# Kernel tuning notes

Hardware: AMD Instinct MI355X
Metric: run time of the kernel (lower is better)

Reference implementation:

```python
import jax, jax.numpy as jnp
import numpy as np

B, T, D, UNITS = 64, 2048, 512, 512


def setup_inputs() -> dict:
    key = jax.random.key(0)
    ks = jax.random.split(key, 6)
    scale = 1.0 / np.sqrt(D)
    return {
        "features": jax.random.normal(ks[0], (B, T, D), dtype=jnp.float32),
        "hidden": jax.random.normal(ks[1], (B, D), dtype=jnp.float32),
        "W1_w": jax.random.normal(ks[2], (D, UNITS), dtype=jnp.float32) * scale,
        "W1_b": jnp.zeros((UNITS,), dtype=jnp.float32),
        "W2_w": jax.random.normal(ks[3], (D, UNITS), dtype=jnp.float32) * scale,
        "W2_b": jnp.zeros((UNITS,), dtype=jnp.float32),
        "V_w": jax.random.normal(ks[4], (UNITS, 1), dtype=jnp.float32) * (1.0 / np.sqrt(UNITS)),
        "V_b": jnp.zeros((1,), dtype=jnp.float32),
    }


def reference(features, hidden, W1_w, W1_b, W2_w, W2_b, V_w, V_b):
    # features: [B, T, D], hidden: [B, D]
    f_proj = jnp.einsum("btd,du->btu", features, W1_w) + W1_b      # [B, T, U]
    h_proj = (hidden @ W2_w + W2_b)[:, None, :]                     # [B, 1, U]
    score = jnp.tanh(f_proj + h_proj) @ V_w + V_b                   # [B, T, 1]
    attn = jax.nn.softmax(score, axis=1)                            # softmax over time
    context = jnp.sum(attn * features, axis=1)                      # [B, D]
    return context
```

## Files before the change

kernel.cpp:

```cpp
#include <hip/hip_runtime.h>
#include <hip/hip_bf16.h>

#define B_DIM 64
#define T_DIM 2048
#define D_DIM 512
#define U_DIM 512

typedef __bf16 bf16x8 __attribute__((ext_vector_type(8)));
typedef float  f32x4  __attribute__((ext_vector_type(4)));
typedef unsigned int u32;

__device__ __forceinline__ void gl_lds16(const __bf16* g, __bf16* l) {
    __builtin_amdgcn_global_load_lds(
        (const __attribute__((address_space(1))) u32*)g,
        (__attribute__((address_space(3))) u32*)l,
        16, 0, 0);
}

__global__ void w1s_kernel(const float* __restrict__ W1w, __bf16* __restrict__ w1s) {
    __shared__ float tile[64][33];
    const int tid = threadIdx.x;
    const int kb2 = blockIdx.x;
    const int ub  = blockIdx.y;
    #pragma unroll
    for (int i = 0; i < 8; ++i) {
        int k = i * 4 + (tid >> 6);
        int u = tid & 63;
        tile[u][k] = W1w[(kb2 * 32 + k) * U_DIM + ub * 64 + u];
    }
    __syncthreads();
    int u_l = tid >> 2;
    int kp  = (tid & 3) * 8;
    bf16x8 w;
    #pragma unroll
    for (int j = 0; j < 8; ++j) w[j] = (__bf16)tile[u_l][kp + j];
    *reinterpret_cast<bf16x8*>(&w1s[kb2 * 16384 + (ub * 64 + u_l) * 32 + kp]) = w;
}

__global__ void hproj_kernel(const float* __restrict__ hidden,
                             const float* __restrict__ W2w,
                             const float* __restrict__ W2b,
                             const float* __restrict__ W1b,
                             float* __restrict__ hp) {
    int b = blockIdx.x;
    int u = blockIdx.y * 256 + threadIdx.x;
    float acc = W2b[u] + W1b[u];
    const float* hrow = hidden + b * D_DIM;
    #pragma unroll 8
    for (int d = 0; d < D_DIM; ++d)
        acc = fmaf(hrow[d], W2w[d * U_DIM + u], acc);
    hp[b * U_DIM + u] = acc;
}

__global__ __launch_bounds__(256, 2) void score_ctx_kernel(
        const float*  __restrict__ features,
        const __bf16* __restrict__ w1s,
        const float*  __restrict__ hp,
        const float*  __restrict__ Vw,
        float*        __restrict__ ctx,
        float*        __restrict__ mv,
        float*        __restrict__ lv) {
    __shared__ __align__(16) char smem[8192 + 65536 + 1024 + 256];
    __bf16* As  = (__bf16*)smem;
    __bf16* Bs  = (__bf16*)(smem + 8192);
    float*  red = (float*)(smem + 8192 + 65536);
    float*  se  = (float*)(smem + 8192 + 65536 + 1024);
    float4* red4 = (float4*)Bs;

    const int tid  = threadIdx.x;
    const int chunk = blockIdx.x;
    const int row0 = chunk * 64;
    const int b    = row0 >> 11;

    const int wn   = tid >> 6;
    const int lane = tid & 63;
    const int l16  = lane & 15;
    const int quad = lane >> 4;

    f32x4 acc[4][8];
    #pragma unroll
    for (int i = 0; i < 4; ++i)
        #pragma unroll
        for (int j = 0; j < 8; ++j)
            acc[i][j] = (f32x4)0.0f;

    const int arow = tid >> 2;
    const int aq   = tid & 3;
    const float* agp = features + (size_t)(row0 + arow) * D_DIM + aq * 8;

    {
        const __bf16* src = w1s + tid * 8;
        #pragma unroll
        for (int c = 0; c < 8; ++c)
            gl_lds16(src + c * 2048, Bs + c * 2048 + tid * 8);
        const float4* s = reinterpret_cast<const float4*>(agp);
        float4 v0 = s[0], v1 = s[1];
        bf16x8 w;
        w[0] = (__bf16)v0.x; w[1] = (__bf16)v0.y; w[2] = (__bf16)v0.z; w[3] = (__bf16)v0.w;
        w[4] = (__bf16)v1.x; w[5] = (__bf16)v1.y; w[6] = (__bf16)v1.z; w[7] = (__bf16)v1.w;
        *reinterpret_cast<bf16x8*>(&As[arow * 32 + aq * 8]) = w;
    }
    __syncthreads();

    #pragma unroll
    for (int p = 0; p < 16; ++p) {
        const int cur = p & 1;
        if (p < 15) {
            const int nxt = cur ^ 1;
            const __bf16* src = w1s + (p + 1) * 16384 + tid * 8;
            __bf16* dst = Bs + nxt * 16384 + tid * 8;
            #pragma unroll
            for (int c = 0; c < 8; ++c)
                gl_lds16(src + c * 2048, dst + c * 2048);
            const float4* s = reinterpret_cast<const float4*>(agp + (p + 1) * 32);
            float4 v0 = s[0], v1 = s[1];
            bf16x8 w;
            w[0] = (__bf16)v0.x; w[1] = (__bf16)v0.y; w[2] = (__bf16)v0.z; w[3] = (__bf16)v0.w;
            w[4] = (__bf16)v1.x; w[5] = (__bf16)v1.y; w[6] = (__bf16)v1.z; w[7] = (__bf16)v1.w;
            *reinterpret_cast<bf16x8*>(&As[nxt * 2048 + arow * 32 + aq * 8]) = w;
        }
        const __bf16* Ap = As + cur * 2048;
        const __bf16* Bp = Bs + cur * 16384;
        bf16x8 af[4], bfr[8];
        #pragma unroll
        for (int mt = 0; mt < 4; ++mt)
            af[mt] = *reinterpret_cast<const bf16x8*>(
                &Ap[(mt * 16 + l16) * 32 + quad * 8]);
        #pragma unroll
        for (int nt = 0; nt < 8; ++nt)
            bfr[nt] = *reinterpret_cast<const bf16x8*>(
                &Bp[(wn * 128 + nt * 16 + l16) * 32 + quad * 8]);
        #pragma unroll
        for (int mt = 0; mt < 4; ++mt)
            #pragma unroll
            for (int nt = 0; nt < 8; ++nt)
                acc[mt][nt] = __builtin_amdgcn_mfma_f32_16x16x32_bf16(
                    af[mt], bfr[nt], acc[mt][nt], 0, 0, 0);
        __syncthreads();
    }

    float hpv[8], vwv[8];
    #pragma unroll
    for (int nt = 0; nt < 8; ++nt) {
        int u = wn * 128 + nt * 16 + l16;
        hpv[nt] = hp[b * U_DIM + u];
        vwv[nt] = Vw[u];
    }
    #pragma unroll
    for (int mt = 0; mt < 4; ++mt) {
        #pragma unroll
        for (int reg = 0; reg < 4; ++reg) {
            float s = 0.0f;
            #pragma unroll
            for (int nt = 0; nt < 8; ++nt) {
                float x = acc[mt][nt][reg] + hpv[nt];
                float e = exp2f(x * 2.88539008f);
                float th = 1.0f - 2.0f * __builtin_amdgcn_rcpf(e + 1.0f);
                s = fmaf(th, vwv[nt], s);
            }
            s += __shfl_xor(s, 1);
            s += __shfl_xor(s, 2);
            s += __shfl_xor(s, 4);
            s += __shfl_xor(s, 8);
            if (l16 == 0)
                red[wn * 64 + mt * 16 + quad * 4 + reg] = s;
        }
    }
    __syncthreads();

    if (tid < 64) {
        float s = red[tid] + red[64 + tid] + red[128 + tid] + red[192 + tid];
        float m = s;
        #pragma unroll
        for (int off = 1; off < 64; off <<= 1) m = fmaxf(m, __shfl_xor(m, off));
        float e = exp2f((s - m) * 1.44269504f);
        se[tid] = e;
        float l = e;
        #pragma unroll
        for (int off = 1; off < 64; off <<= 1) l += __shfl_xor(l, off);
        if (tid == 0) { mv[chunk] = m; lv[chunk] = l; }
    }
    __syncthreads();

    {
        const int col  = tid & 127;
        const int half = tid >> 7;
        const float4* fb = reinterpret_cast<const float4*>(features)
                           + (size_t)row0 * 128 + col;
        float4 a4 = {0.f, 0.f, 0.f, 0.f};
        #pragma unroll 8
        for (int i = 0; i < 32; ++i) {
            int t = half * 32 + i;
            float e = se[t];
            float4 v = fb[(size_t)t * 128];
            a4.x = fmaf(e, v.x, a4.x);
            a4.y = fmaf(e, v.y, a4.y);
            a4.z = fmaf(e, v.z, a4.z);
            a4.w = fmaf(e, v.w, a4.w);
        }
        red4[tid] = a4;
        __syncthreads();
        if (half == 0) {
            float4 v = red4[tid + 128];
            a4 = red4[tid];
            a4.x += v.x; a4.y += v.y; a4.z += v.z; a4.w += v.w;
            reinterpret_cast<float4*>(ctx)[(size_t)chunk * 128 + col] = a4;
        }
    }
}

__global__ void combine_kernel(const float* __restrict__ ctx,
                               const float* __restrict__ mv,
                               const float* __restrict__ lv,
                               float* __restrict__ out) {
    __shared__ float w[32];
    const int b   = blockIdx.x;
    const int tid = threadIdx.x;
    if (tid < 32) {
        float m = mv[b * 32 + tid];
        float M = m;
        #pragma unroll
        for (int off = 1; off < 32; off <<= 1) M = fmaxf(M, __shfl_xor(M, off));
        float wc = exp2f((m - M) * 1.44269504f);
        float l  = lv[b * 32 + tid] * wc;
        #pragma unroll
        for (int off = 1; off < 32; off <<= 1) l += __shfl_xor(l, off);
        w[tid] = wc / l;
    }
    __syncthreads();
    #pragma unroll
    for (int r = 0; r < 2; ++r) {
        int d = r * 256 + tid;
        float s = 0.0f;
        #pragma unroll
        for (int c = 0; c < 32; ++c)
            s = fmaf(ctx[(size_t)(b * 32 + c) * 512 + d], w[c], s);
        out[b * 512 + d] = s;
    }
}

extern "C" void kernel_launch(void* const* d_in, const int* in_sizes, int n_in,
                              void* d_out, int out_size, void* d_ws, size_t ws_size,
                              hipStream_t stream) {
    const float* features = (const float*)d_in[0];
    const float* hidden   = (const float*)d_in[1];
    const float* W1w      = (const float*)d_in[2];
    const float* W1b      = (const float*)d_in[3];
    const float* W2w      = (const float*)d_in[4];
    const float* W2b      = (const float*)d_in[5];
    const float* Vw       = (const float*)d_in[6];

    char* ws = (char*)d_ws;
    __bf16* w1s = (__bf16*)ws;
    float*  hp  = (float*)(ws + (512u << 10));
    float*  ctx = (float*)(ws + (640u << 10));
    float*  mv  = (float*)(ws + (640u << 10) + (4u << 20));
    float*  lv  = (float*)(ws + (640u << 10) + (4u << 20) + 8192u);

    hipLaunchKernelGGL(w1s_kernel, dim3(16, 8), dim3(256), 0, stream, W1w, w1s);
    hipLaunchKernelGGL(hproj_kernel, dim3(B_DIM, 2), dim3(256), 0, stream,
                       hidden, W2w, W2b, W1b, hp);
    hipLaunchKernelGGL(score_ctx_kernel, dim3(2048), dim3(256), 0, stream,
                       features, w1s, hp, Vw, ctx, mv, lv);
    hipLaunchKernelGGL(combine_kernel, dim3(B_DIM), dim3(256), 0, stream,
                       ctx, mv, lv, (float*)d_out);
}
```

Before: 475.8 us.

## Swizzle A/B LDS tiles into MFMA fragment order and prefetch features two stages ahead

The pre-transposed W1 buffer and the LDS tile for the features operand are now stored in MFMA fragment order, so each lane's 16-byte fragment load is contiguous by lane index. This is meant to remove the LDS bank conflicts caused by the old row-major 64-byte stride. Separately, the fp32 feature loads are issued one stage earlier and held in registers, which hides global load latency behind the MFMA work at the cost of more VGPRs.

```diff
diff --git a/kernel.cpp b/kernel.cpp
--- a/kernel.cpp
+++ b/kernel.cpp
@@ -30,11 +30,13 @@
     }
     __syncthreads();
     int u_l = tid >> 2;
-    int kp  = (tid & 3) * 8;
+    int kq  = tid & 3;
     bf16x8 w;
     #pragma unroll
-    for (int j = 0; j < 8; ++j) w[j] = (__bf16)tile[u_l][kp + j];
-    *reinterpret_cast<bf16x8*>(&w1s[kb2 * 16384 + (ub * 64 + u_l) * 32 + kp]) = w;
+    for (int j = 0; j < 8; ++j) w[j] = (__bf16)tile[u_l][kq * 8 + j];
+    int g    = ub * 4 + (u_l >> 4);
+    int lane = kq * 16 + (u_l & 15);
+    *reinterpret_cast<bf16x8*>(&w1s[kb2 * 16384 + g * 512 + lane * 8]) = w;
 }
 
 __global__ void hproj_kernel(const float* __restrict__ hidden,
@@ -87,49 +89,57 @@
     const int arow = tid >> 2;
     const int aq   = tid & 3;
     const float* agp = features + (size_t)(row0 + arow) * D_DIM + aq * 8;
-
+    const int awoff = (arow >> 4) * 512 + aq * 128 + (arow & 15) * 8;
+
+#define CVT_W(V0, V1, W)                                                      \
+    W[0] = (__bf16)V0.x; W[1] = (__bf16)V0.y; W[2] = (__bf16)V0.z;            \
+    W[3] = (__bf16)V0.w; W[4] = (__bf16)V1.x; W[5] = (__bf16)V1.y;            \
+    W[6] = (__bf16)V1.z; W[7] = (__bf16)V1.w;
+
+    float4 ar[2][2];
     {
         const __bf16* src = w1s + tid * 8;
         #pragma unroll
         for (int c = 0; c < 8; ++c)
             gl_lds16(src + c * 2048, Bs + c * 2048 + tid * 8);
-        const float4* s = reinterpret_cast<const float4*>(agp);
-        float4 v0 = s[0], v1 = s[1];
+        const float4* s0 = reinterpret_cast<const float4*>(agp);
+        ar[0][0] = s0[0]; ar[0][1] = s0[1];
         bf16x8 w;
-        w[0] = (__bf16)v0.x; w[1] = (__bf16)v0.y; w[2] = (__bf16)v0.z; w[3] = (__bf16)v0.w;
-        w[4] = (__bf16)v1.x; w[5] = (__bf16)v1.y; w[6] = (__bf16)v1.z; w[7] = (__bf16)v1.w;
-        *reinterpret_cast<bf16x8*>(&As[arow * 32 + aq * 8]) = w;
+        CVT_W(ar[0][0], ar[0][1], w)
+        *reinterpret_cast<bf16x8*>(&As[awoff]) = w;
+        const float4* s1 = reinterpret_cast<const float4*>(agp + 32);
+        ar[1][0] = s1[0]; ar[1][1] = s1[1];
     }
     __syncthreads();
 
     #pragma unroll
     for (int p = 0; p < 16; ++p) {
         const int cur = p & 1;
+        const int nxt = cur ^ 1;
         if (p < 15) {
-            const int nxt = cur ^ 1;
             const __bf16* src = w1s + (p + 1) * 16384 + tid * 8;
             __bf16* dst = Bs + nxt * 16384 + tid * 8;
             #pragma unroll
             for (int c = 0; c < 8; ++c)
                 gl_lds16(src + c * 2048, dst + c * 2048);
-            const float4* s = reinterpret_cast<const float4*>(agp + (p + 1) * 32);
-            float4 v0 = s[0], v1 = s[1];
             bf16x8 w;
-            w[0] = (__bf16)v0.x; w[1] = (__bf16)v0.y; w[2] = (__bf16)v0.z; w[3] = (__bf16)v0.w;
-            w[4] = (__bf16)v1.x; w[5] = (__bf16)v1.y; w[6] = (__bf16)v1.z; w[7] = (__bf16)v1.w;
-            *reinterpret_cast<bf16x8*>(&As[nxt * 2048 + arow * 32 + aq * 8]) = w;
+            CVT_W(ar[nxt][0], ar[nxt][1], w)
+            *reinterpret_cast<bf16x8*>(&As[nxt * 2048 + awoff]) = w;
+        }
+        if (p < 14) {
+            const float4* s = reinterpret_cast<const float4*>(agp + (p + 2) * 32);
+            ar[cur][0] = s[0]; ar[cur][1] = s[1];
         }
         const __bf16* Ap = As + cur * 2048;
         const __bf16* Bp = Bs + cur * 16384;
         bf16x8 af[4], bfr[8];
         #pragma unroll
         for (int mt = 0; mt < 4; ++mt)
-            af[mt] = *reinterpret_cast<const bf16x8*>(
-                &Ap[(mt * 16 + l16) * 32 + quad * 8]);
+            af[mt] = *reinterpret_cast<const bf16x8*>(&Ap[mt * 512 + lane * 8]);
         #pragma unroll
         for (int nt = 0; nt < 8; ++nt)
             bfr[nt] = *reinterpret_cast<const bf16x8*>(
-                &Bp[(wn * 128 + nt * 16 + l16) * 32 + quad * 8]);
+                &Bp[(wn * 8 + nt) * 512 + lane * 8]);
         #pragma unroll
         for (int mt = 0; mt < 4; ++mt)
             #pragma unroll
@@ -138,6 +148,7 @@
                     af[mt], bfr[nt], acc[mt][nt], 0, 0, 0);
         __syncthreads();
     }
+#undef CVT_W
 
     float hpv[8], vwv[8];
     #pragma unroll
```

Measured after the change: 469.2 us. About the same (-1.4%).
